# Optimization experiments

Hardware: AMD Instinct MI355X
Metric: run time of the kernel (lower is better)

## Reference

```python
import jax, jax.numpy as jnp
import numpy as np

N = 100_000        # nodes
F_IN = 1024        # input features
H1, C1 = 8, 8      # layer-1 heads, per-head channels (concat -> 64)
C_OUT = 40         # num classes (layer-2, heads=1, concat=False)
E = 3_200_000      # directed edges (avg degree 32)
NEG_SLOPE = 0.2    # PyG GATConv default leaky_relu slope


def setup_inputs() -> dict:
    key = jax.random.key(0)
    ks = jax.random.split(key, 10)
    x = jax.random.normal(ks[0], (N, F_IN), jnp.float32)
    edge_index = jax.random.randint(ks[1], (2, E), 0, N, dtype=jnp.int32)
    s1 = 1.0 / np.sqrt(F_IN)
    W1 = jax.random.normal(ks[2], (F_IN, H1 * C1), jnp.float32) * s1
    sa = 1.0 / np.sqrt(C1)
    att_src1 = jax.random.normal(ks[3], (H1, C1), jnp.float32) * sa
    att_dst1 = jax.random.normal(ks[4], (H1, C1), jnp.float32) * sa
    b1 = jnp.zeros((H1 * C1,), jnp.float32)
    s2 = 1.0 / np.sqrt(H1 * C1)
    W2 = jax.random.normal(ks[5], (H1 * C1, C_OUT), jnp.float32) * s2
    so = 1.0 / np.sqrt(C_OUT)
    att_src2 = jax.random.normal(ks[6], (1, C_OUT), jnp.float32) * so
    att_dst2 = jax.random.normal(ks[7], (1, C_OUT), jnp.float32) * so
    b2 = jnp.zeros((C_OUT,), jnp.float32)
    return {"x": x, "edge_index": edge_index, "W1": W1, "att_src1": att_src1,
            "att_dst1": att_dst1, "b1": b1, "W2": W2, "att_src2": att_src2,
            "att_dst2": att_dst2, "b2": b2}


def gat_layer(x, src, dst, W, a_src, a_dst, b, heads, ch, concat, n):
    # per-head linear projection: [n, heads, ch]
    xw = (x @ W).reshape(n, heads, ch)
    # per-node attention logits: [n, heads]
    al_src = jnp.einsum('nhc,hc->nh', xw, a_src)
    al_dst = jnp.einsum('nhc,hc->nh', xw, a_dst)
    # per-edge scores (message src -> dst): [e, heads]
    e = jax.nn.leaky_relu(al_src[src] + al_dst[dst], NEG_SLOPE)
    # segment softmax over incoming edges of each dst node
    m = jax.ops.segment_max(e, dst, num_segments=n)          # [n, heads]
    p = jnp.exp(e - m[dst])
    denom = jax.ops.segment_sum(p, dst, num_segments=n)      # [n, heads]
    alpha = p / (denom[dst] + 1e-16)                          # [e, heads]
    # weighted scatter-sum of source features
    out = jax.ops.segment_sum(xw[src] * alpha[:, :, None], dst, num_segments=n)
    out = out.reshape(n, heads * ch) if concat else out.mean(axis=1)
    return out + b


def reference(x, edge_index, W1, att_src1, att_dst1, b1, W2, att_src2, att_dst2, b2):
    n = x.shape[0]
    # PyG GATConv default: add self loops
    loop = jnp.arange(n, dtype=edge_index.dtype)
    src = jnp.concatenate([edge_index[0], loop])
    dst = jnp.concatenate([edge_index[1], loop])
    h = jax.nn.elu(gat_layer(x, src, dst, W1, att_src1, att_dst1, b1, H1, C1, True, n))
    h = gat_layer(h, src, dst, W2, att_src2, att_dst2, b2, 1, C_OUT, False, n)
    return jax.nn.log_softmax(h, axis=1)
```

## Files before the change

### kernel.cpp

```cpp
#include <hip/hip_runtime.h>
#include <hip/hip_bf16.h>
#include <cstdint>
#include <cstddef>

#define F_IN 1024
#define F1 64
#define H1 8
#define C1 8
#define C_OUT 40
#define XW2S 64
#define NEG 0.2f
#define LOG2E 1.442695040888963387f
#define B1 256
#define BSHIFT 8
#define BNODES 256

typedef __attribute__((ext_vector_type(8))) short short8;
typedef __attribute__((ext_vector_type(4))) float f32x4;

static __device__ __forceinline__ unsigned short f2bf(float f) {
  union { float f; unsigned u; } v; v.f = f;
  unsigned r = v.u + 0x7fff + ((v.u >> 16) & 1);
  return (unsigned short)(r >> 16);
}
static __device__ __forceinline__ float bf2f(unsigned short h) {
  union { unsigned u; float f; } v; v.u = ((unsigned)h) << 16; return v.f;
}
static __device__ __forceinline__ unsigned pkbf(float a, float b) {
  union { __hip_bfloat162 h; unsigned u; } c;
  c.h = __float22bfloat162_rn(float2{a, b});
  return c.u;
}
static __device__ __forceinline__ int rfl(int v) {
  return __builtin_amdgcn_readfirstlane(v);
}

__global__ __launch_bounds__(256) void w1cvt_kernel(const float* __restrict__ W1,
                                                    unsigned short* __restrict__ w1t) {
  int i = blockIdx.x * 256 + threadIdx.x;
  int c = i >> 10, k = i & 1023;
  w1t[i] = f2bf(W1[(size_t)k * F1 + c]);
}

__global__ __launch_bounds__(256) void k1_hist_gemm(const float* __restrict__ x,
    const unsigned short* __restrict__ w1t, unsigned short* __restrict__ xw1,
    const int* __restrict__ dst, int* __restrict__ cnt, int n, int e, int nbuck) {
  const int bid = blockIdx.x;
  const int tid = threadIdx.x;
  if (bid < B1) {
    __shared__ int lh[512];
    lh[tid] = 0; lh[tid + 256] = 0;
    __syncthreads();
    int chunk = (e + B1 - 1) / B1;
    int s = bid * chunk, en = min(e, s + chunk);
    for (int i = s + tid; i < en; i += 256) atomicAdd(&lh[dst[i] >> BSHIFT], 1);
    __syncthreads();
    for (int b = tid; b < nbuck; b += 256) cnt[b * B1 + bid] = lh[b];
    return;
  }
  const int gb = bid - B1;
  const int wv = tid >> 6;
  const int l = tid & 63;
  const int lr = l & 15;
  const int lg = l >> 4;
  const int rowBase = gb * 128 + wv * 32;
  int r0 = rowBase + lr, r1 = rowBase + 16 + lr;
  int r0c = r0 < n ? r0 : (n - 1);
  int r1c = r1 < n ? r1 : (n - 1);
  const float* px0 = x + (size_t)r0c * F_IN + lg * 8;
  const float* px1 = x + (size_t)r1c * F_IN + lg * 8;

  f32x4 acc00 = {0.f,0.f,0.f,0.f}, acc01 = acc00, acc02 = acc00, acc03 = acc00;
  f32x4 acc10 = acc00, acc11 = acc00, acc12 = acc00, acc13 = acc00;

#pragma unroll 2
  for (int k0 = 0; k0 < F_IN; k0 += 32) {
    float4 xa0 = *(const float4*)(px0 + k0);
    float4 xb0 = *(const float4*)(px0 + k0 + 4);
    float4 xa1 = *(const float4*)(px1 + k0);
    float4 xb1 = *(const float4*)(px1 + k0 + 4);
    union { short8 s; unsigned u[4]; } a0, a1;
    a0.u[0] = pkbf(xa0.x, xa0.y); a0.u[1] = pkbf(xa0.z, xa0.w);
    a0.u[2] = pkbf(xb0.x, xb0.y); a0.u[3] = pkbf(xb0.z, xb0.w);
    a1.u[0] = pkbf(xa1.x, xa1.y); a1.u[1] = pkbf(xa1.z, xa1.w);
    a1.u[2] = pkbf(xb1.x, xb1.y); a1.u[3] = pkbf(xb1.z, xb1.w);
    const size_t kOff = (size_t)(k0 + lg * 8);
    short8 b0 = *(const short8*)(w1t + (size_t)(0 * 16 + lr) * F_IN + kOff);
    short8 b1 = *(const short8*)(w1t + (size_t)(1 * 16 + lr) * F_IN + kOff);
    short8 b2 = *(const short8*)(w1t + (size_t)(2 * 16 + lr) * F_IN + kOff);
    short8 b3 = *(const short8*)(w1t + (size_t)(3 * 16 + lr) * F_IN + kOff);
    acc00 = __builtin_amdgcn_mfma_f32_16x16x32_bf16(a0.s, b0, acc00, 0, 0, 0);
    acc01 = __builtin_amdgcn_mfma_f32_16x16x32_bf16(a0.s, b1, acc01, 0, 0, 0);
    acc02 = __builtin_amdgcn_mfma_f32_16x16x32_bf16(a0.s, b2, acc02, 0, 0, 0);
    acc03 = __builtin_amdgcn_mfma_f32_16x16x32_bf16(a0.s, b3, acc03, 0, 0, 0);
    acc10 = __builtin_amdgcn_mfma_f32_16x16x32_bf16(a1.s, b0, acc10, 0, 0, 0);
    acc11 = __builtin_amdgcn_mfma_f32_16x16x32_bf16(a1.s, b1, acc11, 0, 0, 0);
    acc12 = __builtin_amdgcn_mfma_f32_16x16x32_bf16(a1.s, b2, acc12, 0, 0, 0);
    acc13 = __builtin_amdgcn_mfma_f32_16x16x32_bf16(a1.s, b3, acc13, 0, 0, 0);
  }

#pragma unroll
  for (int r = 0; r < 4; ++r) {
    int o0 = rowBase + lg * 4 + r;
    if (o0 < n) {
      unsigned short* po = xw1 + (size_t)o0 * F1 + lr;
      po[0]  = f2bf(acc00[r]);
      po[16] = f2bf(acc01[r]);
      po[32] = f2bf(acc02[r]);
      po[48] = f2bf(acc03[r]);
    }
    int o1 = rowBase + 16 + lg * 4 + r;
    if (o1 < n) {
      unsigned short* po = xw1 + (size_t)o1 * F1 + lr;
      po[0]  = f2bf(acc10[r]);
      po[16] = f2bf(acc11[r]);
      po[32] = f2bf(acc12[r]);
      po[48] = f2bf(acc13[r]);
    }
  }
}

__global__ __launch_bounds__(256) void k2_scan_al1(const int* __restrict__ in,
    int* __restrict__ excl, int* __restrict__ bsum, int len, int nbScan,
    const unsigned short* __restrict__ xw1, const float* __restrict__ asrc,
    const float* __restrict__ adst, float* __restrict__ al_src,
    float* __restrict__ al_dst, int n) {
  const int bid = blockIdx.x;
  const int tid = threadIdx.x;
  if (bid < nbScan) {
    __shared__ int s[256];
    int gid = bid * 256 + tid;
    int v = gid < len ? in[gid] : 0;
    s[tid] = v;
    __syncthreads();
    for (int ofs = 1; ofs < 256; ofs <<= 1) {
      int t = (tid >= ofs) ? s[tid - ofs] : 0;
      __syncthreads();
      s[tid] += t;
      __syncthreads();
    }
    if (gid < len) excl[gid] = s[tid] - v;
    if (tid == 255) bsum[bid] = s[255];
    return;
  }
  int id = (bid - nbScan) * 256 + tid;
  if (id >= n * H1) return;
  int node = id >> 3, h = id & 7;
  union { short8 s; unsigned short u[8]; } rowv;
  rowv.s = *(const short8*)(xw1 + (size_t)node * F1 + h * C1);
  float s = 0.f, d = 0.f;
#pragma unroll
  for (int c = 0; c < C1; ++c) {
    float v = bf2f(rowv.u[c]);
    s += v * asrc[h * C1 + c];
    d += v * adst[h * C1 + c];
  }
  al_src[id] = s * LOG2E;
  al_dst[id] = d * LOG2E;
}

__global__ __launch_bounds__(1024) void scan2_kernel(int* __restrict__ bsum, int nb) {
  __shared__ int s[1024];
  int tid = threadIdx.x;
  int v = tid < nb ? bsum[tid] : 0;
  s[tid] = v;
  __syncthreads();
  for (int ofs = 1; ofs < 1024; ofs <<= 1) {
    int t = (tid >= ofs) ? s[tid - ofs] : 0;
    __syncthreads();
    s[tid] += t;
    __syncthreads();
  }
  if (tid < nb) bsum[tid] = s[tid] - v;
}

__global__ __launch_bounds__(256) void binscatter_kernel(const int* __restrict__ src,
    const int* __restrict__ dst, const int* __restrict__ cntS,
    const int* __restrict__ bsum, unsigned* __restrict__ binned, int e, int nbuck) {
  __shared__ int lcur[512];
  int tid = threadIdx.x, blk = blockIdx.x;
  for (int b = tid; b < nbuck; b += 256) lcur[b] = cntS[b * B1 + blk] + bsum[b];
  __syncthreads();
  int chunk = (e + gridDim.x - 1) / gridDim.x;
  int s = blk * chunk, en = min(e, s + chunk);
  for (int i = s + tid; i < en; i += 256) {
    int d = dst[i];
    int pos = atomicAdd(&lcur[d >> BSHIFT], 1);
    binned[pos] = ((unsigned)(d & (BNODES - 1)) << 23) | (unsigned)src[i];
  }
}

__global__ __launch_bounds__(256) void bucket_csr_kernel(const unsigned* __restrict__ binned,
    const int* __restrict__ bsum, int* __restrict__ deg, int* __restrict__ off,
    int* __restrict__ csr, int e, int n, int nbuck) {
  int q = blockIdx.x, tid = threadIdx.x;
  int eBase = bsum[q];
  int eEnd = (q + 1 < nbuck) ? bsum[q + 1] : e;
  __shared__ int nh[BNODES], sc[BNODES], cu[BNODES];
  nh[tid] = 0;
  __syncthreads();
  for (int i = eBase + tid; i < eEnd; i += 256) atomicAdd(&nh[binned[i] >> 23], 1);
  __syncthreads();
  int v = nh[tid];
  sc[tid] = v;
  __syncthreads();
  for (int ofs = 1; ofs < BNODES; ofs <<= 1) {
    int t = (tid >= ofs) ? sc[tid - ofs] : 0;
    __syncthreads();
    sc[tid] += t;
    __syncthreads();
  }
  int ex = sc[tid] - v;
  cu[tid] = ex;
  int node0 = q * BNODES + tid;
  if (node0 < n) { deg[node0] = v; off[node0] = eBase + ex; }
  __syncthreads();
  for (int i = eBase + tid; i < eEnd; i += 256) {
    unsigned w = binned[i];
    int pos = eBase + atomicAdd(&cu[w >> 23], 1);
    csr[pos] = (int)(w & 0x7FFFFF);
  }
}

__global__ __launch_bounds__(256) void gat1_agg(const unsigned short* __restrict__ xw1,
    const float* __restrict__ al_src, const float* __restrict__ al_dst,
    const int* __restrict__ csr, const int* __restrict__ off, const int* __restrict__ deg,
    const float* __restrict__ b1, float* __restrict__ h1, int n) {
  const int node = rfl((int)((blockIdx.x * blockDim.x + threadIdx.x) >> 6));
  if (node >= n) return;
  const int lane = threadIdx.x & 63;
  const int half = lane >> 5;
  const int c2 = lane & 31;
  const int h = c2 >> 2;
  const int base = rfl(off[node]);
  const int cnt = rfl(deg[node]);
  const float adst = al_dst[node * H1 + h];
  const int* __restrict__ csrp = csr + base;
  const char* xwB = (const char*)xw1;
  const char* alB = (const char*)al_src;
  const int cOff = c2 << 2;
  const int hOff = h << 2;

  float acc0 = 0.f, acc1 = 0.f, l = 0.f;

#define PAIR_BODY(wv_, av_) { \
    float t = (av_) + adst; \
    float sc = fmaxf(t, NEG * t); \
    float p = __builtin_amdgcn_exp2f(sc); \
    acc0 = fmaf(p, bf2f((unsigned short)((wv_) & 0xffffu)), acc0); \
    acc1 = fmaf(p, bf2f((unsigned short)((wv_) >> 16)), acc1); \
    l += p; }

  int it = 0;
  for (; it + 16 <= cnt; it += 16) {
    int xo[8];
#pragma unroll
    for (int jp = 0; jp < 8; ++jp) {
      int s0 = rfl(csrp[it + 2 * jp]) << 7;
      int s1 = rfl(csrp[it + 2 * jp + 1]) << 7;
      xo[jp] = half ? s1 : s0;
    }
    unsigned wv[8]; float av[8];
#pragma unroll
    for (int jp = 0; jp < 8; ++jp) {
      wv[jp] = *(const unsigned*)(xwB + xo[jp] + cOff);
      av[jp] = *(const float*)(alB + (xo[jp] >> 2) + hOff);
    }
#pragma unroll
    for (int jp = 0; jp < 8; ++jp) PAIR_BODY(wv[jp], av[jp]);
  }
  for (; it + 2 <= cnt; it += 2) {
    int s0 = rfl(csrp[it]) << 7;
    int s1 = rfl(csrp[it + 1]) << 7;
    int bs = half ? s1 : s0;
    unsigned w = *(const unsigned*)(xwB + bs + cOff);
    float av = *(const float*)(alB + (bs >> 2) + hOff);
    PAIR_BODY(w, av);
  }
  {
    const bool odd = (it < cnt);
    int sA = odd ? rfl(csrp[it]) : node;
    int bs = (half ? node : sA) << 7;
    unsigned w = *(const unsigned*)(xwB + bs + cOff);
    float av = *(const float*)(alB + (bs >> 2) + hOff);
    float t = av + adst;
    float sc = fmaxf(t, NEG * t);
    float p = __builtin_amdgcn_exp2f(sc);
    if (!odd && half) p = 0.f;
    acc0 = fmaf(p, bf2f((unsigned short)(w & 0xffffu)), acc0);
    acc1 = fmaf(p, bf2f((unsigned short)(w >> 16)), acc1);
    l += p;
  }
#undef PAIR_BODY

  acc0 += __shfl_xor(acc0, 32);
  acc1 += __shfl_xor(acc1, 32);
  l    += __shfl_xor(l, 32);
  if (half == 0) {
    float inv = 1.f / (l + 1e-16f);
    float2 bv = *(const float2*)(b1 + (c2 << 1));
    float o0 = acc0 * inv + bv.x;
    float o1 = acc1 * inv + bv.y;
    o0 = o0 > 0.f ? o0 : __expf(o0) - 1.f;
    o1 = o1 > 0.f ? o1 : __expf(o1) - 1.f;
    *(float2*)(h1 + (size_t)node * F1 + (c2 << 1)) = make_float2(o0, o1);
  }
}

__global__ __launch_bounds__(256) void gemm2_kernel(const float* __restrict__ h1,
    const float* __restrict__ W2, const float* __restrict__ asrc,
    const float* __restrict__ adst, unsigned short* __restrict__ xw2,
    float* __restrict__ alS2, float* __restrict__ alD2, int n) {
  __shared__ float ws[F1 * C_OUT];
  __shared__ float wsa[C_OUT], wsd[C_OUT];
  int tid = threadIdx.x;
  for (int i = tid; i < F1 * C_OUT; i += 256) ws[i] = W2[i];
  if (tid < C_OUT) { wsa[tid] = asrc[tid]; wsd[tid] = adst[tid]; }
  __syncthreads();
  int node = blockIdx.x * 256 + tid;
  if (node >= n) return;
  const float4* row4 = (const float4*)(h1 + (size_t)node * F1);
  float acc[C_OUT];
#pragma unroll
  for (int j = 0; j < C_OUT; ++j) acc[j] = 0.f;
#pragma unroll 2
  for (int k4 = 0; k4 < 16; ++k4) {
    float4 xv = row4[k4];
    const float* w0 = &ws[(4 * k4 + 0) * C_OUT];
    const float* w1 = &ws[(4 * k4 + 1) * C_OUT];
    const float* w2 = &ws[(4 * k4 + 2) * C_OUT];
    const float* w3 = &ws[(4 * k4 + 3) * C_OUT];
#pragma unroll
    for (int j = 0; j < C_OUT; j += 4) {
      float4 v0 = *(const float4*)(w0 + j);
      float4 v1 = *(const float4*)(w1 + j);
      float4 v2 = *(const float4*)(w2 + j);
      float4 v3 = *(const float4*)(w3 + j);
      acc[j + 0] += xv.x * v0.x + xv.y * v1.x + xv.z * v2.x + xv.w * v3.x;
      acc[j + 1] += xv.x * v0.y + xv.y * v1.y + xv.z * v2.y + xv.w * v3.y;
      acc[j + 2] += xv.x * v0.z + xv.y * v1.z + xv.z * v2.z + xv.w * v3.z;
      acc[j + 3] += xv.x * v0.w + xv.y * v1.w + xv.z * v2.w + xv.w * v3.w;
    }
  }
  float s = 0.f, d = 0.f;
#pragma unroll
  for (int j = 0; j < C_OUT; ++j) { s += acc[j] * wsa[j]; d += acc[j] * wsd[j]; }
  alS2[node] = s * LOG2E;
  alD2[node] = d * LOG2E;
  unsigned short* orow = xw2 + (size_t)node * XW2S;
#pragma unroll
  for (int j = 0; j < C_OUT; j += 4) {
    ushort4 o;
    o.x = f2bf(acc[j + 0]); o.y = f2bf(acc[j + 1]);
    o.z = f2bf(acc[j + 2]); o.w = f2bf(acc[j + 3]);
    *(ushort4*)(orow + j) = o;
  }
}

__global__ __launch_bounds__(256) void gat2_agg(const unsigned short* __restrict__ xw2,
    const float* __restrict__ alS, const float* __restrict__ alD,
    const int* __restrict__ csr, const int* __restrict__ off, const int* __restrict__ deg,
    const float* __restrict__ b2, float* __restrict__ out, int n) {
  const int node = rfl((int)((blockIdx.x * blockDim.x + threadIdx.x) >> 6));
  if (node >= n) return;
  const int lane = threadIdx.x & 63;
  const int half = lane >> 5;
  const int c2 = lane & 31;
  const bool act = c2 < 20;
  const int c2r = act ? c2 : 0;
  const int base = rfl(off[node]);
  const int cnt = rfl(deg[node]);
  const float adst = alD[node];
  const int* __restrict__ csrp = csr + base;
  const char* xwB = (const char*)xw2;
  const char* alB = (const char*)alS;
  const int cOff = c2r << 2;

  float acc0 = 0.f, acc1 = 0.f, l = 0.f;

#define PAIR_BODY2(wv_, av_) { \
    float t = (av_) + adst; \
    float sc = fmaxf(t, NEG * t); \
    float p = __builtin_amdgcn_exp2f(sc); \
    acc0 = fmaf(p, bf2f((unsigned short)((wv_) & 0xffffu)), acc0); \
    acc1 = fmaf(p, bf2f((unsigned short)((wv_) >> 16)), acc1); \
    l += p; }

  int it = 0;
  for (; it + 16 <= cnt; it += 16) {
    int xo[8];
#pragma unroll
    for (int jp = 0; jp < 8; ++jp) {
      int s0 = rfl(csrp[it + 2 * jp]) << 7;
      int s1 = rfl(csrp[it + 2 * jp + 1]) << 7;
      xo[jp] = half ? s1 : s0;
    }
    unsigned wv[8]; float av[8];
#pragma unroll
    for (int jp = 0; jp < 8; ++jp) {
      wv[jp] = *(const unsigned*)(xwB + xo[jp] + cOff);
      av[jp] = *(const float*)(alB + (xo[jp] >> 5));
    }
#pragma unroll
    for (int jp = 0; jp < 8; ++jp) PAIR_BODY2(wv[jp], av[jp]);
  }
  for (; it + 2 <= cnt; it += 2) {
    int s0 = rfl(csrp[it]) << 7;
    int s1 = rfl(csrp[it + 1]) << 7;
    int bs = half ? s1 : s0;
    unsigned w = *(const unsigned*)(xwB + bs + cOff);
    float av = *(const float*)(alB + (bs >> 5));
    PAIR_BODY2(w, av);
  }
  {
    const bool odd = (it < cnt);
    int sA = odd ? rfl(csrp[it]) : node;
    int bs = (half ? node : sA) << 7;
    unsigned w = *(const unsigned*)(xwB + bs + cOff);
    float av = *(const float*)(alB + (bs >> 5));
    float t = av + adst;
    float sc = fmaxf(t, NEG * t);
    float p = __builtin_amdgcn_exp2f(sc);
    if (!odd && half) p = 0.f;
    acc0 = fmaf(p, bf2f((unsigned short)(w & 0xffffu)), acc0);
    acc1 = fmaf(p, bf2f((unsigned short)(w >> 16)), acc1);
    l += p;
  }
#undef PAIR_BODY2

  acc0 += __shfl_xor(acc0, 32);
  acc1 += __shfl_xor(acc1, 32);
  l    += __shfl_xor(l, 32);

  float inv = 1.f / (l + 1e-16f);
  float v0 = -1e30f, v1 = -1e30f;
  if (act) {
    float2 bv = *(const float2*)(b2 + (c2 << 1));
    v0 = acc0 * inv + bv.x;
    v1 = acc1 * inv + bv.y;
  }
  float mx = fmaxf(v0, v1);
#pragma unroll
  for (int mask = 1; mask <= 16; mask <<= 1) mx = fmaxf(mx, __shfl_xor(mx, mask));
  float e0 = act ? __expf(v0 - mx) : 0.f;
  float e1 = act ? __expf(v1 - mx) : 0.f;
  float sum = e0 + e1;
#pragma unroll
  for (int mask = 1; mask <= 16; mask <<= 1) sum += __shfl_xor(sum, mask);
  if (half == 0 && act) {
    float ls = __logf(sum);
    *(float2*)(out + (size_t)node * C_OUT + (c2 << 1)) =
        make_float2(v0 - mx - ls, v1 - mx - ls);
  }
}

extern "C" void kernel_launch(void* const* d_in, const int* in_sizes, int n_in,
                              void* d_out, int out_size, void* d_ws, size_t ws_size,
                              hipStream_t stream) {
  const float* x   = (const float*)d_in[0];
  const int*   ei  = (const int*)d_in[1];
  const float* W1  = (const float*)d_in[2];
  const float* as1 = (const float*)d_in[3];
  const float* ad1 = (const float*)d_in[4];
  const float* b1  = (const float*)d_in[5];
  const float* W2  = (const float*)d_in[6];
  const float* as2 = (const float*)d_in[7];
  const float* ad2 = (const float*)d_in[8];
  const float* b2  = (const float*)d_in[9];
  float* out = (float*)d_out;

  const int n = in_sizes[0] / F_IN;
  const int e = in_sizes[1] / 2;
  const int* srcIdx = ei;
  const int* dstIdx = ei + e;
  const int nbuck = (n + BNODES - 1) >> BSHIFT;
  const int clen = nbuck * B1;

  char* p = (char*)d_ws;
  auto take = [&](size_t bytes) {
    char* q = p;
    p += (bytes + 255) & ~(size_t)255;
    return q;
  };
  unsigned short* xw1 = (unsigned short*)take((size_t)n * F1 * 2);
  float* h1           = (float*)take((size_t)n * F1 * 4);
  unsigned short* xw2 = (unsigned short*)take((size_t)n * XW2S * 2);
  unsigned short* w1t = (unsigned short*)take((size_t)F_IN * F1 * 2);
  float* alS1 = (float*)take((size_t)n * H1 * 4);
  float* alD1 = (float*)take((size_t)n * H1 * 4);
  float* alS2 = (float*)take((size_t)n * 4);
  float* alD2 = (float*)take((size_t)n * 4);
  int* deg  = (int*)take((size_t)n * 4);
  int* offb = (int*)take((size_t)n * 4);
  int* cnt  = (int*)take((size_t)clen * 4);
  int* cntS = (int*)take((size_t)clen * 4);
  int* bsum = (int*)take(4096);
  unsigned* binned = (unsigned*)take((size_t)e * 4);
  int* csr  = (int*)take((size_t)e * 4);

  dim3 b256(256);
  const int gB = (n + 127) / 128;
  const int alBlocks = (n * H1 + 255) / 256;
  int nbScan = (clen + 255) / 256;

  w1cvt_kernel<<<dim3((F_IN * F1) / 256), b256, 0, stream>>>(W1, w1t);
  k1_hist_gemm<<<dim3(B1 + gB), b256, 0, stream>>>(x, w1t, xw1, dstIdx, cnt, n, e, nbuck);
  k2_scan_al1<<<dim3(nbScan + alBlocks), b256, 0, stream>>>(cnt, cntS, bsum, clen,
      nbScan, xw1, as1, ad1, alS1, alD1, n);
  scan2_kernel<<<dim3(1), dim3(1024), 0, stream>>>(bsum, nbScan);
  binscatter_kernel<<<dim3(B1), b256, 0, stream>>>(srcIdx, dstIdx, cntS, bsum, binned, e, nbuck);
  bucket_csr_kernel<<<dim3(nbuck), b256, 0, stream>>>(binned, bsum, deg, offb, csr, e, n, nbuck);

  gat1_agg<<<dim3((n + 3) / 4), b256, 0, stream>>>(xw1, alS1, alD1, csr, offb, deg, b1, h1, n);
  gemm2_kernel<<<dim3((n + 255) / 256), b256, 0, stream>>>(h1, W2, as2, ad2, xw2, alS2, alD2, n);
  gat2_agg<<<dim3((n + 3) / 4), b256, 0, stream>>>(xw2, alS2, alD2, csr, offb, deg, b2, out, n);
}
```

Measured before the change: 405.4 us.

## Fuse layer-1 aggregation with layer-2 projection to drop h1 buffer

```diff
diff --git a/kernel.cpp b/kernel.cpp
--- a/kernel.cpp
+++ b/kernel.cpp
@@ -222,26 +222,38 @@
   }
 }
 
-__global__ __launch_bounds__(256) void gat1_agg(const unsigned short* __restrict__ xw1,
+__global__ __launch_bounds__(256) void gat1_fused(const unsigned short* __restrict__ xw1,
     const float* __restrict__ al_src, const float* __restrict__ al_dst,
     const int* __restrict__ csr, const int* __restrict__ off, const int* __restrict__ deg,
-    const float* __restrict__ b1, float* __restrict__ h1, int n) {
-  const int node = rfl((int)((blockIdx.x * blockDim.x + threadIdx.x) >> 6));
-  if (node >= n) return;
-  const int lane = threadIdx.x & 63;
+    const float* __restrict__ b1, const float* __restrict__ W2,
+    const float* __restrict__ asrc2, const float* __restrict__ adst2,
+    unsigned short* __restrict__ xw2, float* __restrict__ alS2,
+    float* __restrict__ alD2, int n) {
+  __shared__ float ws[F1 * C_OUT];
+  __shared__ float wsa[C_OUT], wsd[C_OUT];
+  __shared__ float h1s[4][F1];
+  const int tid = threadIdx.x;
+  for (int i = tid; i < F1 * C_OUT; i += 256) ws[i] = W2[i];
+  if (tid < C_OUT) { wsa[tid] = asrc2[tid]; wsd[tid] = adst2[tid]; }
+
+  const int wv = tid >> 6;
+  const int node = blockIdx.x * 4 + wv;
+  const int lane = tid & 63;
   const int half = lane >> 5;
   const int c2 = lane & 31;
-  const int h = c2 >> 2;
-  const int base = rfl(off[node]);
-  const int cnt = rfl(deg[node]);
-  const float adst = al_dst[node * H1 + h];
-  const int* __restrict__ csrp = csr + base;
-  const char* xwB = (const char*)xw1;
-  const char* alB = (const char*)al_src;
-  const int cOff = c2 << 2;
-  const int hOff = h << 2;
-
-  float acc0 = 0.f, acc1 = 0.f, l = 0.f;
+
+  if (node < n) {
+    const int h = c2 >> 2;
+    const int base = rfl(off[node]);
+    const int cnt = rfl(deg[node]);
+    const float adst = al_dst[node * H1 + h];
+    const int* __restrict__ csrp = csr + base;
+    const char* xwB = (const char*)xw1;
+    const char* alB = (const char*)al_src;
+    const int cOff = c2 << 2;
+    const int hOff = h << 2;
+
+    float acc0 = 0.f, acc1 = 0.f, l = 0.f;
 
 #define PAIR_BODY(wv_, av_) { \
     float t = (av_) + adst; \
@@ -251,110 +263,85 @@
     acc1 = fmaf(p, bf2f((unsigned short)((wv_) >> 16)), acc1); \
     l += p; }
 
-  int it = 0;
-  for (; it + 16 <= cnt; it += 16) {
-    int xo[8];
-#pragma unroll
-    for (int jp = 0; jp < 8; ++jp) {
-      int s0 = rfl(csrp[it + 2 * jp]) << 7;
-      int s1 = rfl(csrp[it + 2 * jp + 1]) << 7;
-      xo[jp] = half ? s1 : s0;
-    }
-    unsigned wv[8]; float av[8];
-#pragma unroll
-    for (int jp = 0; jp < 8; ++jp) {
-      wv[jp] = *(const unsigned*)(xwB + xo[jp] + cOff);
-      av[jp] = *(const float*)(alB + (xo[jp] >> 2) + hOff);
-    }
-#pragma unroll
-    for (int jp = 0; jp < 8; ++jp) PAIR_BODY(wv[jp], av[jp]);
-  }
-  for (; it + 2 <= cnt; it += 2) {
-    int s0 = rfl(csrp[it]) << 7;
-    int s1 = rfl(csrp[it + 1]) << 7;
-    int bs = half ? s1 : s0;
-    unsigned w = *(const unsigned*)(xwB + bs + cOff);
-    float av = *(const float*)(alB + (bs >> 2) + hOff);
-    PAIR_BODY(w, av);
-  }
-  {
-    const bool odd = (it < cnt);
-    int sA = odd ? rfl(csrp[it]) : node;
-    int bs = (half ? node : sA) << 7;
-    unsigned w = *(const unsigned*)(xwB + bs + cOff);
-    float av = *(const float*)(alB + (bs >> 2) + hOff);
-    float t = av + adst;
-    float sc = fmaxf(t, NEG * t);
-    float p = __builtin_amdgcn_exp2f(sc);
-    if (!odd && half) p = 0.f;
-    acc0 = fmaf(p, bf2f((unsigned short)(w & 0xffffu)), acc0);
-    acc1 = fmaf(p, bf2f((unsigned short)(w >> 16)), acc1);
-    l += p;
-  }
+    int it = 0;
+    for (; it + 16 <= cnt; it += 16) {
+      int xo[8];
+#pragma unroll
+      for (int jp = 0; jp < 8; ++jp) {
+        int s0 = rfl(csrp[it + 2 * jp]) << 7;
+        int s1 = rfl(csrp[it + 2 * jp + 1]) << 7;
+        xo[jp] = half ? s1 : s0;
+      }
+      unsigned wvv[8]; float av[8];
+#pragma unroll
+      for (int jp = 0; jp < 8; ++jp) {
+        wvv[jp] = *(const unsigned*)(xwB + xo[jp] + cOff);
+        av[jp] = *(const float*)(alB + (xo[jp] >> 2) + hOff);
+      }
+#pragma unroll
+      for (int jp = 0; jp < 8; ++jp) PAIR_BODY(wvv[jp], av[jp]);
+    }
+    for (; it + 2 <= cnt; it += 2) {
+      int s0 = rfl(csrp[it]) << 7;
+      int s1 = rfl(csrp[it + 1]) << 7;
+      int bs = half ? s1 : s0;
+      unsigned w = *(const unsigned*)(xwB + bs + cOff);
+      float av = *(const float*)(alB + (bs >> 2) + hOff);
+      PAIR_BODY(w, av);
+    }
+    {
+      const bool odd = (it < cnt);
+      int sA = odd ? rfl(csrp[it]) : node;
+      int bs = (half ? node : sA) << 7;
+      unsigned w = *(const unsigned*)(xwB + bs + cOff);
+      float av = *(const float*)(alB + (bs >> 2) + hOff);
+      float t = av + adst;
+      float sc = fmaxf(t, NEG * t);
+      float p = __builtin_amdgcn_exp2f(sc);
+      if (!odd && half) p = 0.f;
+      acc0 = fmaf(p, bf2f((unsigned short)(w & 0xffffu)), acc0);
+      acc1 = fmaf(p, bf2f((unsigned short)(w >> 16)), acc1);
+      l += p;
+    }
 #undef PAIR_BODY
 
-  acc0 += __shfl_xor(acc0, 32);
-  acc1 += __shfl_xor(acc1, 32);
-  l    += __shfl_xor(l, 32);
-  if (half == 0) {
-    float inv = 1.f / (l + 1e-16f);
-    float2 bv = *(const float2*)(b1 + (c2 << 1));
-    float o0 = acc0 * inv + bv.x;
-    float o1 = acc1 * inv + bv.y;
-    o0 = o0 > 0.f ? o0 : __expf(o0) - 1.f;
-    o1 = o1 > 0.f ? o1 : __expf(o1) - 1.f;
-    *(float2*)(h1 + (size_t)node * F1 + (c2 << 1)) = make_float2(o0, o1);
-  }
-}
-
-__global__ __launch_bounds__(256) void gemm2_kernel(const float* __restrict__ h1,
-    const float* __restrict__ W2, const float* __restrict__ asrc,
-    const float* __restrict__ adst, unsigned short* __restrict__ xw2,
-    float* __restrict__ alS2, float* __restrict__ alD2, int n) {
-  __shared__ float ws[F1 * C_OUT];
-  __shared__ float wsa[C_OUT], wsd[C_OUT];
-  int tid = threadIdx.x;
-  for (int i = tid; i < F1 * C_OUT; i += 256) ws[i] = W2[i];
-  if (tid < C_OUT) { wsa[tid] = asrc[tid]; wsd[tid] = adst[tid]; }
-  __syncthreads();
-  int node = blockIdx.x * 256 + tid;
-  if (node >= n) return;
-  const float4* row4 = (const float4*)(h1 + (size_t)node * F1);
-  float acc[C_OUT];
-#pragma unroll
-  for (int j = 0; j < C_OUT; ++j) acc[j] = 0.f;
-#pragma unroll 2
-  for (int k4 = 0; k4 < 16; ++k4) {
-    float4 xv = row4[k4];
-    const float* w0 = &ws[(4 * k4 + 0) * C_OUT];
-    const float* w1 = &ws[(4 * k4 + 1) * C_OUT];
-    const float* w2 = &ws[(4 * k4 + 2) * C_OUT];
-    const float* w3 = &ws[(4 * k4 + 3) * C_OUT];
-#pragma unroll
-    for (int j = 0; j < C_OUT; j += 4) {
-      float4 v0 = *(const float4*)(w0 + j);
-      float4 v1 = *(const float4*)(w1 + j);
-      float4 v2 = *(const float4*)(w2 + j);
-      float4 v3 = *(const float4*)(w3 + j);
-      acc[j + 0] += xv.x * v0.x + xv.y * v1.x + xv.z * v2.x + xv.w * v3.x;
-      acc[j + 1] += xv.x * v0.y + xv.y * v1.y + xv.z * v2.y + xv.w * v3.y;
-      acc[j + 2] += xv.x * v0.z + xv.y * v1.z + xv.z * v2.z + xv.w * v3.z;
-      acc[j + 3] += xv.x * v0.w + xv.y * v1.w + xv.z * v2.w + xv.w * v3.w;
-    }
-  }
-  float s = 0.f, d = 0.f;
-#pragma unroll
-  for (int j = 0; j < C_OUT; ++j) { s += acc[j] * wsa[j]; d += acc[j] * wsd[j]; }
-  alS2[node] = s * LOG2E;
-  alD2[node] = d * LOG2E;
-  unsigned short* orow = xw2 + (size_t)node * XW2S;
-#pragma unroll
-  for (int j = 0; j < C_OUT; j += 4) {
-    ushort4 o;
-    o.x = f2bf(acc[j + 0]); o.y = f2bf(acc[j + 1]);
-    o.z = f2bf(acc[j + 2]); o.w = f2bf(acc[j + 3]);
-    *(ushort4*)(orow + j) = o;
-  }
+    acc0 += __shfl_xor(acc0, 32);
+    acc1 += __shfl_xor(acc1, 32);
+    l    += __shfl_xor(l, 32);
+    if (half == 0) {
+      float inv = 1.f / (l + 1e-16f);
+      float2 bv = *(const float2*)(b1 + (c2 << 1));
+      float o0 = acc0 * inv + bv.x;
+      float o1 = acc1 * inv + bv.y;
+      o0 = o0 > 0.f ? o0 : __expf(o0) - 1.f;
+      o1 = o1 > 0.f ? o1 : __expf(o1) - 1.f;
+      h1s[wv][c2 * 2 + 0] = o0;
+      h1s[wv][c2 * 2 + 1] = o1;
+    }
+  }
+  __syncthreads();
+
+  const int nd = wv;
+  const int j = lane;
+  const int node2 = blockIdx.x * 4 + nd;
+  if (node2 >= n) return;
+  float acc = 0.f;
+  if (j < C_OUT) {
+#pragma unroll 8
+    for (int k = 0; k < F1; ++k) acc = fmaf(h1s[nd][k], ws[k * C_OUT + j], acc);
+  }
+  float sv = (j < C_OUT) ? acc * wsa[j] : 0.f;
+  float dv = (j < C_OUT) ? acc * wsd[j] : 0.f;
+#pragma unroll
+  for (int mask = 1; mask <= 32; mask <<= 1) {
+    sv += __shfl_xor(sv, mask);
+    dv += __shfl_xor(dv, mask);
+  }
+  if (j == 0) {
+    alS2[node2] = sv * LOG2E;
+    alD2[node2] = dv * LOG2E;
+  }
+  if (j < C_OUT) xw2[(size_t)node2 * XW2S + j] = f2bf(acc);
 }
 
 __global__ __launch_bounds__(256) void gat2_agg(const unsigned short* __restrict__ xw2,
@@ -483,7 +470,6 @@
     return q;
   };
   unsigned short* xw1 = (unsigned short*)take((size_t)n * F1 * 2);
-  float* h1           = (float*)take((size_t)n * F1 * 4);
   unsigned short* xw2 = (unsigned short*)take((size_t)n * XW2S * 2);
   unsigned short* w1t = (unsigned short*)take((size_t)F_IN * F1 * 2);
   float* alS1 = (float*)take((size_t)n * H1 * 4);
@@ -511,7 +497,7 @@
   binscatter_kernel<<<dim3(B1), b256, 0, stream>>>(srcIdx, dstIdx, cntS, bsum, binned, e, nbuck);
   bucket_csr_kernel<<<dim3(nbuck), b256, 0, stream>>>(binned, bsum, deg, offb, csr, e, n, nbuck);
 
-  gat1_agg<<<dim3((n + 3) / 4), b256, 0, stream>>>(xw1, alS1, alD1, csr, offb, deg, b1, h1, n);
-  gemm2_kernel<<<dim3((n + 255) / 256), b256, 0, stream>>>(h1, W2, as2, ad2, xw2, alS2, alD2, n);
+  gat1_fused<<<dim3((n + 3) / 4), b256, 0, stream>>>(xw1, alS1, alD1, csr, offb, deg,
+      b1, W2, as2, ad2, xw2, alS2, alD2, n);
   gat2_agg<<<dim3((n + 3) / 4), b256, 0, stream>>>(xw2, alS2, alD2, csr, offb, deg, b2, out, n);
 }
```

Result: slower. 423.4 us (+4.4%).
